# Performance work log

Measured on AMD Instinct MI355X. Metric: run time of the kernel, lower is better.

## Reference

```python
import jax, jax.numpy as jnp
import numpy as np

B, N, C = 16, 4096, 64
M, K, R = 1024, 32, 0.2
EPS = 1e-5  # BatchNorm eps (eval mode: running_mean=0, running_var=1)


def setup_inputs() -> dict:
    key = jax.random.key(0)
    ks = jax.random.split(key, 8)
    s = 0.05
    return {
        "points": jax.random.normal(ks[0], (B, 3, N), dtype=jnp.float32),
        "features": jax.random.normal(ks[1], (B, C, N), dtype=jnp.float32),
        "w1": jax.random.normal(ks[2], (64, 3 + C), dtype=jnp.float32) * s,
        "b1": jnp.zeros((64,), jnp.float32),
        "g1": jnp.ones((64,), jnp.float32),
        "be1": jnp.zeros((64,), jnp.float32),
        "w2": jax.random.normal(ks[3], (64, 64), dtype=jnp.float32) * s,
        "b2": jnp.zeros((64,), jnp.float32),
        "g2": jnp.ones((64,), jnp.float32),
        "be2": jnp.zeros((64,), jnp.float32),
        "w3": jax.random.normal(ks[4], (128, 64), dtype=jnp.float32) * s,
        "b3": jnp.zeros((128,), jnp.float32),
        "g3": jnp.ones((128,), jnp.float32),
        "be3": jnp.zeros((128,), jnp.float32),
    }


def farthest_point_sampling(pts, m):
    """pts: [B,N,3] -> indices [B,m] (iterative FPS, first point = index 0)."""
    b, n, _ = pts.shape

    def step(carry, _):
        dist, last = carry  # dist [b,n], last [b]
        lastp = jnp.take_along_axis(pts, last[:, None, None], axis=1)  # [b,1,3]
        d = jnp.sum((pts - lastp) ** 2, axis=-1)  # [b,n]
        dist = jnp.minimum(dist, d)
        nxt = jnp.argmax(dist, axis=1).astype(jnp.int32)
        return (dist, nxt), last

    init = (jnp.full((b, n), 1e10, pts.dtype), jnp.zeros((b,), jnp.int32))
    _, idx = jax.lax.scan(step, init, None, length=m)
    return idx.T  # [b,m]


def ball_query(pts, centroids, k, radius):
    """pts [B,N,3], centroids [B,M,3] -> neighbor indices [B,M,K].
    Takes the first k points (by index) within radius; pads with the first hit,
    matching the PointNet++ CUDA ball_query semantics."""
    n = pts.shape[1]
    p2 = jnp.sum(pts ** 2, -1)  # [B,N]
    c2 = jnp.sum(centroids ** 2, -1)  # [B,M]
    d2 = c2[:, :, None] + p2[:, None, :] - 2.0 * jnp.einsum("bmd,bnd->bmn", centroids, pts)
    ar = jnp.arange(n, dtype=jnp.int32)
    key = jnp.where(d2 <= radius * radius, ar[None, None, :], n)  # [B,M,N]
    idx = jnp.sort(key, axis=-1)[..., :k]  # first k in-radius indices (or n)
    first = idx[..., :1]  # centroid itself is always a hit (d2=0)
    idx = jnp.where(idx < n, idx, first)
    return jnp.clip(idx, 0, n - 1)


def _mlp_block(x, w, bias, g, be):
    # 1x1 Conv2d + BatchNorm (eval: mean=0, var=1) + ReLU, x: [B,M,K,Cin]
    y = jnp.einsum("oc,bmkc->bmko", w, x) + bias
    y = y * (g / jnp.sqrt(1.0 + EPS)) + be
    return jax.nn.relu(y)


def reference(points, features, w1, b1, g1, be1, w2, b2, g2, be2, w3, b3, g3, be3):
    pts = jnp.transpose(points, (0, 2, 1))  # [B,N,3]
    feats = jnp.transpose(features, (0, 2, 1))  # [B,N,C]
    b = pts.shape[0]

    cidx = farthest_point_sampling(pts, M)  # [B,M]
    bidx = jnp.arange(b)[:, None]
    cent = pts[bidx, cidx]  # [B,M,3]

    nidx = ball_query(pts, cent, K, R)  # [B,M,K]
    bidx2 = jnp.arange(b)[:, None, None]
    gpts = pts[bidx2, nidx]  # [B,M,K,3]
    gfeat = feats[bidx2, nidx]  # [B,M,K,C]
    local = gpts - cent[:, :, None, :]  # local coords
    x = jnp.concatenate([local, gfeat], axis=-1)  # [B,M,K,3+C]

    x = _mlp_block(x, w1, b1, g1, be1)
    x = _mlp_block(x, w2, b2, g2, be2)
    x = _mlp_block(x, w3, b3, g3, be3)

    out = jnp.max(x, axis=2)  # max over K samples -> [B,M,Cout]
    centroids = jnp.transpose(cent, (0, 2, 1))  # [B,3,M]
    out = jnp.transpose(out, (0, 2, 1))  # [B,Cout,M]
    return centroids, out
```

## Files before the change

kernel.cpp:

```cpp
#include <hip/hip_runtime.h>
#include <math.h>

#define NPTS 4096
#define MC   1024
#define KNB  32

typedef __attribute__((ext_vector_type(8))) short bf16x8;
typedef __attribute__((ext_vector_type(4))) float f32x4;

__device__ __forceinline__ unsigned short f2bf(float f) {
  unsigned int u = __float_as_uint(f);
  u = u + 0x7fffu + ((u >> 16) & 1u);
  return (unsigned short)(u >> 16);
}

template <int CTRL>
__device__ __forceinline__ float dpp_max(float v) {
  int o = __builtin_amdgcn_update_dpp(__float_as_int(v), __float_as_int(v), CTRL, 0xF, 0xF, false);
  return fmaxf(v, __int_as_float(o));
}

struct FpsShared {
  float sx[NPTS], sy[NPTS], sz[NPTS];
  unsigned long long skey[2][4];
  float slog[3][MC];
};
struct TransShared {
  float tile[64][65];
};

__global__ __launch_bounds__(256, 1) void fused_pre(
    const float* __restrict__ points, const float* __restrict__ feats,
    const float* __restrict__ w1, const float* __restrict__ w2,
    const float* __restrict__ w3,
    unsigned short* __restrict__ featsT, unsigned short* __restrict__ wpack,
    float* __restrict__ out_cent) {
  __shared__ union { FpsShared f; TransShared tr; } S;
  const int blk = blockIdx.x;
  const int t = threadIdx.x;

  if (blk < 16) {
    const int b = blk;
    const int w = t >> 6;
    const float* pb = points + (size_t)b * 3 * NPTS;

    float fx[16], fy[16], fz[16], dist[16];
#pragma unroll
    for (int k = 0; k < 4; ++k) {
      float4 X = ((const float4*)pb)[k * 256 + t];
      float4 Y = ((const float4*)(pb + NPTS))[k * 256 + t];
      float4 Z = ((const float4*)(pb + 2 * NPTS))[k * 256 + t];
      ((float4*)S.f.sx)[k * 256 + t] = X;
      ((float4*)S.f.sy)[k * 256 + t] = Y;
      ((float4*)S.f.sz)[k * 256 + t] = Z;
      fx[k * 4 + 0] = X.x; fx[k * 4 + 1] = X.y; fx[k * 4 + 2] = X.z; fx[k * 4 + 3] = X.w;
      fy[k * 4 + 0] = Y.x; fy[k * 4 + 1] = Y.y; fy[k * 4 + 2] = Y.z; fy[k * 4 + 3] = Y.w;
      fz[k * 4 + 0] = Z.x; fz[k * 4 + 1] = Z.y; fz[k * 4 + 2] = Z.z; fz[k * 4 + 3] = Z.w;
    }
#pragma unroll
    for (int j = 0; j < 16; ++j) dist[j] = 1e10f;
    __syncthreads();

    float lx = S.f.sx[0], ly = S.f.sy[0], lz = S.f.sz[0];

    for (int i = 0; i < MC; ++i) {
      if (t == 0) { S.f.slog[0][i] = lx; S.f.slog[1][i] = ly; S.f.slog[2][i] = lz; }
      if (i == MC - 1) break;

      float m = -1.0f;
#pragma unroll
      for (int j = 0; j < 16; ++j) {
        float dx = __fsub_rn(fx[j], lx);
        float dy = __fsub_rn(fy[j], ly);
        float dz = __fsub_rn(fz[j], lz);
        float d  = __fadd_rn(__fadd_rn(__fmul_rn(dx, dx), __fmul_rn(dy, dy)), __fmul_rn(dz, dz));
        float dm = fminf(dist[j], d);
        dist[j] = dm;
        m = fmaxf(m, dm);
      }

      m = dpp_max<0x111>(m);
      m = dpp_max<0x112>(m);
      m = dpp_max<0x114>(m);
      m = dpp_max<0x118>(m);
      m = dpp_max<0x142>(m);
      m = dpp_max<0x143>(m);
      const float wv = __int_as_float(__builtin_amdgcn_readlane(__float_as_int(m), 63));

      unsigned long long mk[4][4];
#pragma unroll
      for (int k = 0; k < 4; ++k) {
        mk[k][0] = __ballot(dist[k * 4 + 0] == wv);
        mk[k][1] = __ballot(dist[k * 4 + 1] == wv);
        mk[k][2] = __ballot(dist[k * 4 + 2] == wv);
        mk[k][3] = __ballot(dist[k * 4 + 3] == wv);
      }
      unsigned long long s0 = 0, s1 = 0, s2 = 0, s3 = 0, anyk = 0;
      int sk = -1;
#pragma unroll
      for (int k = 0; k < 4; ++k) {
        unsigned long long a = mk[k][0] | mk[k][1] | mk[k][2] | mk[k][3];
        if (sk < 0 && a != 0ull) {
          sk = k; anyk = a;
          s0 = mk[k][0]; s1 = mk[k][1]; s2 = mk[k][2]; s3 = mk[k][3];
        }
      }
      const int l = __builtin_ctzll(anyk);
      const unsigned long long bit = 1ull << l;
      const int c = (s0 & bit) ? 0 : (s1 & bit) ? 1 : (s2 & bit) ? 2 : 3;
      const int selIdx = sk * 1024 + 256 * w + 4 * l + c;

      const int nb = i & 1;
      if ((t & 63) == 0)
        S.f.skey[nb][w] = ((unsigned long long)__float_as_uint(wv) << 32) | (unsigned int)~selIdx;
      __syncthreads();

      unsigned long long k0 = S.f.skey[nb][0], k1 = S.f.skey[nb][1];
      unsigned long long k2 = S.f.skey[nb][2], k3 = S.f.skey[nb][3];
      unsigned long long ka = (k0 > k1) ? k0 : k1;
      unsigned long long kb = (k2 > k3) ? k2 : k3;
      unsigned long long km = (ka > kb) ? ka : kb;
      const int sel = (int)(~(unsigned int)km);
      lx = S.f.sx[sel]; ly = S.f.sy[sel]; lz = S.f.sz[sel];
    }
    __syncthreads();
    float* oc = out_cent + (size_t)b * 3 * MC;
#pragma unroll
    for (int k = 0; k < 12; ++k) {
      int idx = t + k * 256;
      oc[idx] = ((const float*)S.f.slog)[idx];
    }
  } else if (blk < 16 + 1024) {
    const int rel = blk - 16;
    const int b = rel >> 6;
    const int n0 = (rel & 63) * 64;
    const float* src = feats + (size_t)b * 64 * NPTS;
    {
      const int n = t & 63, cbase = t >> 6;
#pragma unroll
      for (int j = 0; j < 16; ++j) {
        int cc = cbase + j * 4;
        S.tr.tile[cc][n] = src[(size_t)cc * NPTS + n0 + n];
      }
    }
    __syncthreads();
    {
      const int cc = t & 63, nbase = t >> 6;
      unsigned short* dst = featsT + ((size_t)b * NPTS + n0) * 64;
#pragma unroll
      for (int j = 0; j < 16; ++j) {
        int n = nbase + j * 4;
        dst[(size_t)n * 64 + cc] = f2bf(S.tr.tile[cc][n]);
      }
    }
  } else {
    const int f = (blk - (16 + 1024)) * 4 + (t >> 6);
    const int lane = t & 63;
    if (f < 36) {
      int layer, kt, nt;
      if (f < 12)      { layer = 0; kt = f >> 2;        nt = f & 3; }
      else if (f < 20) { layer = 1; kt = (f - 12) >> 2; nt = (f - 12) & 3; }
      else             { layer = 2; kt = (f - 20) >> 3; nt = (f - 20) & 7; }
      const int o = nt * 16 + (lane & 15);
      unsigned short* dst = wpack + ((size_t)f * 64 + lane) * 8;
#pragma unroll
      for (int j = 0; j < 8; ++j) {
        int k = kt * 32 + (lane >> 4) * 8 + j;
        float x = 0.0f;
        if (layer == 0)      { if (k < 67) { int cin = (k < 64) ? (k + 3) : (k - 64); x = w1[o * 67 + cin]; } }
        else if (layer == 1) { x = w2[o * 64 + k]; }
        else                 { x = w3[o * 64 + k]; }
        dst[j] = f2bf(x);
      }
    }
  }
}

__global__ __launch_bounds__(256) void ball_query_kernel(const float* __restrict__ points,
                                                         const float* __restrict__ cent,
                                                         int* __restrict__ nidx) {
  __shared__ float sx[NPTS], sy[NPTS], sz[NPTS];
  __shared__ int lists[4][KNB];
  const int b  = blockIdx.x >> 4;
  const int cb = blockIdx.x & 15;
  const int t = threadIdx.x;
  const float* pb = points + (size_t)b * 3 * NPTS;
#pragma unroll
  for (int j = 0; j < 4; ++j) {
    int i4 = t + j * 256;
    ((float4*)sx)[i4] = ((const float4*)pb)[i4];
    ((float4*)sy)[i4] = ((const float4*)(pb + NPTS))[i4];
    ((float4*)sz)[i4] = ((const float4*)(pb + 2 * NPTS))[i4];
  }
  __syncthreads();
  const int w = t >> 6, lane = t & 63;
  const float R2 = (float)(0.2 * 0.2);
  const float* cbp = cent + (size_t)b * 3 * MC;
  for (int cm = 0; cm < 16; ++cm) {
    const int m  = cb * 64 + w * 16 + cm;
    const int bm = b * MC + m;
    const float cx = cbp[m], cy = cbp[MC + m], cz = cbp[2 * MC + m];
    const float c2 = __fadd_rn(__fadd_rn(__fmul_rn(cx, cx), __fmul_rn(cy, cy)), __fmul_rn(cz, cz));
    int cnt = 0;
    for (int ch = 0; ch < 64; ++ch) {
      const int n = ch * 64 + lane;
      float x = sx[n], y = sy[n], z = sz[n];
      float p2  = __fadd_rn(__fadd_rn(__fmul_rn(x, x),  __fmul_rn(y, y)),  __fmul_rn(z, z));
      float dot = __fadd_rn(__fadd_rn(__fmul_rn(cx, x), __fmul_rn(cy, y)), __fmul_rn(cz, z));
      float d2  = __fsub_rn(__fadd_rn(c2, p2), __fmul_rn(2.0f, dot));
      bool hit = (d2 <= R2);
      unsigned long long msk = __ballot(hit);
      if (hit) {
        int pos = cnt + __popcll(msk & ((1ull << lane) - 1ull));
        if (pos < KNB) lists[w][pos] = n;
      }
      cnt += __popcll(msk);
      if (cnt >= KNB) break;
    }
    if (lane < KNB) {
      int first = lists[w][0];
      int v = (lane < cnt) ? lists[w][lane] : first;
      nidx[(size_t)bm * KNB + lane] = v;
    }
  }
}

__global__ __launch_bounds__(256) void mlp_kernel(
    const float* __restrict__ points,
    const float* __restrict__ cent,
    const int* __restrict__ nidx,
    const unsigned short* __restrict__ featsT,
    const unsigned short* __restrict__ wpack,
    const float* __restrict__ b1, const float* __restrict__ g1, const float* __restrict__ be1,
    const float* __restrict__ b2, const float* __restrict__ g2, const float* __restrict__ be2,
    const float* __restrict__ b3, const float* __restrict__ g3, const float* __restrict__ be3,
    float* __restrict__ out) {
  __shared__ __align__(16) unsigned short Hs[4][2][32 * 72];
  __shared__ __align__(16) float obuf[128 * 20];
  const int t = threadIdx.x;
  const int w = t >> 6, lane = t & 63;
  const int r = lane & 15, q = lane >> 4;
  const float inv_s = 1.0f / sqrtf(1.0f + 1e-5f);

  float pb1[4], ps1[4], pe1[4], pb2[4], ps2[4], pe2[4], pb3[8], ps3[8], pe3[8];
#pragma unroll
  for (int nt = 0; nt < 4; ++nt) {
    int o = nt * 16 + r;
    pb1[nt] = b1[o]; ps1[nt] = g1[o] * inv_s; pe1[nt] = be1[o];
    pb2[nt] = b2[o]; ps2[nt] = g2[o] * inv_s; pe2[nt] = be2[o];
  }
#pragma unroll
  for (int nt = 0; nt < 8; ++nt) {
    int o = nt * 16 + r;
    pb3[nt] = b3[o]; ps3[nt] = g3[o] * inv_s; pe3[nt] = be3[o];
  }
  const int bm0 = blockIdx.x * 16;
  const int b   = bm0 >> 10;
  const int m0  = bm0 & 1023;
  const float* ptsb = points + (size_t)b * 3 * NPTS;
  const float* cbp  = cent + (size_t)b * 3 * MC;

  for (int it = 0; it < 4; ++it) {
    const int ml = it * 4 + w;
    const int bm = bm0 + ml;
    const int m  = bm & 1023;
    const int n0 = nidx[(size_t)bm * KNB + r];
    const int n1 = nidx[(size_t)bm * KNB + 16 + r];
    const float cx = cbp[m], cy = cbp[MC + m], cz = cbp[2 * MC + m];

    bf16x8 aF[2][2];
#pragma unroll
    for (int mt = 0; mt < 2; ++mt) {
      int n = mt ? n1 : n0;
      const unsigned short* rowp = featsT + ((size_t)b * NPTS + n) * 64 + q * 8;
      aF[mt][0] = *(const bf16x8*)(rowp);
      aF[mt][1] = *(const bf16x8*)(rowp + 32);
    }
    bf16x8 aL[2];
#pragma unroll
    for (int mt = 0; mt < 2; ++mt) {
      bf16x8 a = {0, 0, 0, 0, 0, 0, 0, 0};
      if (q == 0) {
        int n = mt ? n1 : n0;
        a[0] = (short)f2bf(ptsb[n] - cx);
        a[1] = (short)f2bf(ptsb[NPTS + n] - cy);
        a[2] = (short)f2bf(ptsb[2 * NPTS + n] - cz);
      }
      aL[mt] = a;
    }
    f32x4 acc1[2][4];
#pragma unroll
    for (int mt = 0; mt < 2; ++mt)
#pragma unroll
      for (int nt = 0; nt < 4; ++nt) acc1[mt][nt] = (f32x4){0.f, 0.f, 0.f, 0.f};
#pragma unroll
    for (int kt = 0; kt < 3; ++kt) {
#pragma unroll
      for (int nt = 0; nt < 4; ++nt) {
        bf16x8 wf = *(const bf16x8*)(wpack + ((size_t)(kt * 4 + nt) * 64 + lane) * 8);
#pragma unroll
        for (int mt = 0; mt < 2; ++mt) {
          bf16x8 a = (kt < 2) ? aF[mt][kt] : aL[mt];
          acc1[mt][nt] = __builtin_amdgcn_mfma_f32_16x16x32_bf16(a, wf, acc1[mt][nt], 0, 0, 0);
        }
      }
    }
#pragma unroll
    for (int mt = 0; mt < 2; ++mt)
#pragma unroll
      for (int nt = 0; nt < 4; ++nt)
#pragma unroll
        for (int rr = 0; rr < 4; ++rr) {
          float y = (acc1[mt][nt][rr] + pb1[nt]) * ps1[nt] + pe1[nt];
          y = fmaxf(y, 0.0f);
          Hs[w][0][(mt * 16 + q * 4 + rr) * 72 + nt * 16 + r] = f2bf(y);
        }
    __threadfence_block();

    f32x4 acc2[2][4];
#pragma unroll
    for (int mt = 0; mt < 2; ++mt)
#pragma unroll
      for (int nt = 0; nt < 4; ++nt) acc2[mt][nt] = (f32x4){0.f, 0.f, 0.f, 0.f};
#pragma unroll
    for (int kt = 0; kt < 2; ++kt) {
      bf16x8 a0 = *(const bf16x8*)&Hs[w][0][(0 * 16 + r) * 72 + kt * 32 + q * 8];
      bf16x8 a1 = *(const bf16x8*)&Hs[w][0][(1 * 16 + r) * 72 + kt * 32 + q * 8];
#pragma unroll
      for (int nt = 0; nt < 4; ++nt) {
        bf16x8 wf = *(const bf16x8*)(wpack + ((size_t)(12 + kt * 4 + nt) * 64 + lane) * 8);
        acc2[0][nt] = __builtin_amdgcn_mfma_f32_16x16x32_bf16(a0, wf, acc2[0][nt], 0, 0, 0);
        acc2[1][nt] = __builtin_amdgcn_mfma_f32_16x16x32_bf16(a1, wf, acc2[1][nt], 0, 0, 0);
      }
    }
#pragma unroll
    for (int mt = 0; mt < 2; ++mt)
#pragma unroll
      for (int nt = 0; nt < 4; ++nt)
#pragma unroll
        for (int rr = 0; rr < 4; ++rr) {
          float y = (acc2[mt][nt][rr] + pb2[nt]) * ps2[nt] + pe2[nt];
          y = fmaxf(y, 0.0f);
          Hs[w][1][(mt * 16 + q * 4 + rr) * 72 + nt * 16 + r] = f2bf(y);
        }
    __threadfence_block();

    f32x4 acc3[2][8];
#pragma unroll
    for (int mt = 0; mt < 2; ++mt)
#pragma unroll
      for (int nt = 0; nt < 8; ++nt) acc3[mt][nt] = (f32x4){0.f, 0.f, 0.f, 0.f};
#pragma unroll
    for (int kt = 0; kt < 2; ++kt) {
      bf16x8 a0 = *(const bf16x8*)&Hs[w][1][(0 * 16 + r) * 72 + kt * 32 + q * 8];
      bf16x8 a1 = *(const bf16x8*)&Hs[w][1][(1 * 16 + r) * 72 + kt * 32 + q * 8];
#pragma unroll
      for (int nt = 0; nt < 8; ++nt) {
        bf16x8 wf = *(const bf16x8*)(wpack + ((size_t)(20 + kt * 8 + nt) * 64 + lane) * 8);
        acc3[0][nt] = __builtin_amdgcn_mfma_f32_16x16x32_bf16(a0, wf, acc3[0][nt], 0, 0, 0);
        acc3[1][nt] = __builtin_amdgcn_mfma_f32_16x16x32_bf16(a1, wf, acc3[1][nt], 0, 0, 0);
      }
    }
#pragma unroll
    for (int nt = 0; nt < 8; ++nt) {
      float pm = 0.0f;
#pragma unroll
      for (int mt = 0; mt < 2; ++mt)
#pragma unroll
        for (int rr = 0; rr < 4; ++rr) {
          float y = (acc3[mt][nt][rr] + pb3[nt]) * ps3[nt] + pe3[nt];
          y = fmaxf(y, 0.0f);
          pm = fmaxf(pm, y);
        }
      pm = fmaxf(pm, __shfl_xor(pm, 16));
      pm = fmaxf(pm, __shfl_xor(pm, 32));
      if (q == 0) obuf[(nt * 16 + r) * 20 + ml] = pm;
    }
    __threadfence_block();
  }
  __syncthreads();
  {
    const int ch = t >> 1, mh = (t & 1) * 8;
    float4 u0 = *(const float4*)&obuf[ch * 20 + mh];
    float4 u1 = *(const float4*)&obuf[ch * 20 + mh + 4];
    float* outp = out + ((size_t)b * 128 + ch) * 1024 + m0 + mh;
    *(float4*)(outp)     = u0;
    *(float4*)(outp + 4) = u1;
  }
}

extern "C" void kernel_launch(void* const* d_in, const int* in_sizes, int n_in,
                              void* d_out, int out_size, void* d_ws, size_t ws_size,
                              hipStream_t stream) {
  (void)in_sizes; (void)n_in; (void)out_size; (void)ws_size;
  const float* points   = (const float*)d_in[0];
  const float* features = (const float*)d_in[1];
  const float* w1  = (const float*)d_in[2];
  const float* b1  = (const float*)d_in[3];
  const float* g1  = (const float*)d_in[4];
  const float* be1 = (const float*)d_in[5];
  const float* w2  = (const float*)d_in[6];
  const float* b2  = (const float*)d_in[7];
  const float* g2  = (const float*)d_in[8];
  const float* be2 = (const float*)d_in[9];
  const float* w3  = (const float*)d_in[10];
  const float* b3  = (const float*)d_in[11];
  const float* g3  = (const float*)d_in[12];
  const float* be3 = (const float*)d_in[13];

  float* outc = (float*)d_out;
  float* outf = outc + 16 * 3 * 1024;

  char* ws = (char*)d_ws;
  int*            nidx    = (int*)(ws);
  unsigned short* featsT  = (unsigned short*)(ws + 0x200000);
  unsigned short* wpack   = (unsigned short*)(ws + 0xA00000);

  fused_pre<<<16 + 1024 + 9, 256, 0, stream>>>(points, features, w1, w2, w3,
                                               featsT, wpack, outc);
  ball_query_kernel<<<256, 256, 0, stream>>>(points, outc, nidx);
  mlp_kernel<<<1024, 256, 0, stream>>>(points, outc, nidx, featsT, wpack,
                                       b1, g1, be1, b2, g2, be2, b3, g3, be3, outf);
}
```

Before: 979.7 us.

## Publish winner coordinates with FPS keys and use packed fp32 distance math

In the FPS loop, the winning lane of each wave now selects its own point coordinates from registers and writes them to shared memory next to its argmax key. After the barrier every thread picks the winning coordinates directly, so the dependent shared-memory lookup by index is gone and the full point copy in LDS is no longer needed. The distance computation is also rewritten with two-wide float vectors so the compiler can emit packed fp32 ops, with contraction disabled to keep rounding identical. The cost is a 16-way register select per iteration and a wider shared-memory write per wave.

```diff
diff --git a/kernel.cpp b/kernel.cpp
--- a/kernel.cpp
+++ b/kernel.cpp
@@ -7,6 +7,7 @@
 
 typedef __attribute__((ext_vector_type(8))) short bf16x8;
 typedef __attribute__((ext_vector_type(4))) float f32x4;
+typedef __attribute__((ext_vector_type(2))) float f32x2;
 
 __device__ __forceinline__ unsigned short f2bf(float f) {
   unsigned int u = __float_as_uint(f);
@@ -21,8 +22,8 @@
 }
 
 struct FpsShared {
-  float sx[NPTS], sy[NPTS], sz[NPTS];
   unsigned long long skey[2][4];
+  float4 scoord[2][4];
   float slog[3][MC];
 };
 struct TransShared {
@@ -41,7 +42,7 @@
 
   if (blk < 16) {
     const int b = blk;
-    const int w = t >> 6;
+    const int w = t >> 6, lane = t & 63;
     const float* pb = points + (size_t)b * 3 * NPTS;
 
     float fx[16], fy[16], fz[16], dist[16];
@@ -50,33 +51,40 @@
       float4 X = ((const float4*)pb)[k * 256 + t];
       float4 Y = ((const float4*)(pb + NPTS))[k * 256 + t];
       float4 Z = ((const float4*)(pb + 2 * NPTS))[k * 256 + t];
-      ((float4*)S.f.sx)[k * 256 + t] = X;
-      ((float4*)S.f.sy)[k * 256 + t] = Y;
-      ((float4*)S.f.sz)[k * 256 + t] = Z;
       fx[k * 4 + 0] = X.x; fx[k * 4 + 1] = X.y; fx[k * 4 + 2] = X.z; fx[k * 4 + 3] = X.w;
       fy[k * 4 + 0] = Y.x; fy[k * 4 + 1] = Y.y; fy[k * 4 + 2] = Y.z; fy[k * 4 + 3] = Y.w;
       fz[k * 4 + 0] = Z.x; fz[k * 4 + 1] = Z.y; fz[k * 4 + 2] = Z.z; fz[k * 4 + 3] = Z.w;
     }
 #pragma unroll
     for (int j = 0; j < 16; ++j) dist[j] = 1e10f;
-    __syncthreads();
-
-    float lx = S.f.sx[0], ly = S.f.sy[0], lz = S.f.sz[0];
+
+    float lx = pb[0], ly = pb[NPTS], lz = pb[2 * NPTS];
 
     for (int i = 0; i < MC; ++i) {
       if (t == 0) { S.f.slog[0][i] = lx; S.f.slog[1][i] = ly; S.f.slog[2][i] = lz; }
       if (i == MC - 1) break;
 
       float m = -1.0f;
-#pragma unroll
-      for (int j = 0; j < 16; ++j) {
-        float dx = __fsub_rn(fx[j], lx);
-        float dy = __fsub_rn(fy[j], ly);
-        float dz = __fsub_rn(fz[j], lz);
-        float d  = __fadd_rn(__fadd_rn(__fmul_rn(dx, dx), __fmul_rn(dy, dy)), __fmul_rn(dz, dz));
-        float dm = fminf(dist[j], d);
-        dist[j] = dm;
-        m = fmaxf(m, dm);
+      {
+#pragma clang fp contract(off)
+        const f32x2 Lx = (f32x2){lx, lx};
+        const f32x2 Ly = (f32x2){ly, ly};
+        const f32x2 Lz = (f32x2){lz, lz};
+#pragma unroll
+        for (int h = 0; h < 8; ++h) {
+          f32x2 px = (f32x2){fx[2 * h], fx[2 * h + 1]};
+          f32x2 py = (f32x2){fy[2 * h], fy[2 * h + 1]};
+          f32x2 pz = (f32x2){fz[2 * h], fz[2 * h + 1]};
+          f32x2 dx = px - Lx;
+          f32x2 dy = py - Ly;
+          f32x2 dz = pz - Lz;
+          f32x2 d = (dx * dx + dy * dy) + dz * dz;
+          float a0 = fminf(dist[2 * h], d.x);
+          float a1 = fminf(dist[2 * h + 1], d.y);
+          dist[2 * h] = a0;
+          dist[2 * h + 1] = a1;
+          m = fmaxf(m, fmaxf(a0, a1));
+        }
       }
 
       m = dpp_max<0x111>(m);
@@ -110,18 +118,34 @@
       const int c = (s0 & bit) ? 0 : (s1 & bit) ? 1 : (s2 & bit) ? 2 : 3;
       const int selIdx = sk * 1024 + 256 * w + 4 * l + c;
 
+      const int j_sel = sk * 4 + c;
+      float ex = fx[0], ey = fy[0], ez = fz[0];
+#pragma unroll
+      for (int j = 1; j < 16; ++j) {
+        const bool h = (j_sel == j);
+        ex = h ? fx[j] : ex;
+        ey = h ? fy[j] : ey;
+        ez = h ? fz[j] : ez;
+      }
+
       const int nb = i & 1;
-      if ((t & 63) == 0)
-        S.f.skey[nb][w] = ((unsigned long long)__float_as_uint(wv) << 32) | (unsigned int)~selIdx;
+      if (lane == l) {
+        S.f.skey[nb][w] =
+            ((unsigned long long)__float_as_uint(wv) << 32) | (unsigned int)~selIdx;
+        S.f.scoord[nb][w] = make_float4(ex, ey, ez, 0.0f);
+      }
       __syncthreads();
 
       unsigned long long k0 = S.f.skey[nb][0], k1 = S.f.skey[nb][1];
       unsigned long long k2 = S.f.skey[nb][2], k3 = S.f.skey[nb][3];
-      unsigned long long ka = (k0 > k1) ? k0 : k1;
-      unsigned long long kb = (k2 > k3) ? k2 : k3;
-      unsigned long long km = (ka > kb) ? ka : kb;
-      const int sel = (int)(~(unsigned int)km);
-      lx = S.f.sx[sel]; ly = S.f.sy[sel]; lz = S.f.sz[sel];
+      float4 c0 = S.f.scoord[nb][0], c1 = S.f.scoord[nb][1];
+      float4 c2 = S.f.scoord[nb][2], c3 = S.f.scoord[nb][3];
+      unsigned long long ka = k0; float4 ca = c0;
+      if (k1 > ka) { ka = k1; ca = c1; }
+      unsigned long long kb = k2; float4 cb = c2;
+      if (k3 > kb) { kb = k3; cb = c3; }
+      if (kb > ka) { ca = cb; }
+      lx = ca.x; ly = ca.y; lz = ca.z;
     }
     __syncthreads();
     float* oc = out_cent + (size_t)b * 3 * MC;
```

Measured after the change: 1.447 ms. +47.7%, slower.

## Fuse ball query into MLP kernel, keeping neighbor indices in registers

Applied to the files above, without the earlier changes.

Merges the ball query and MLP kernels into one: each block stages its batch's points into shared memory, computes neighbor lists for its 16 centroids, and builds the local coordinate inputs directly from shared memory. This removes one kernel launch, the global neighbor-index buffer round trip, and global gathers of point coordinates. In exchange every MLP block reloads all point coordinates for its batch, and the larger shared-memory union can limit occupancy.

```diff
diff --git a/kernel.cpp b/kernel.cpp
--- a/kernel.cpp
+++ b/kernel.cpp
@@ -176,35 +176,54 @@
   }
 }
 
-__global__ __launch_bounds__(256) void ball_query_kernel(const float* __restrict__ points,
-                                                         const float* __restrict__ cent,
-                                                         int* __restrict__ nidx) {
-  __shared__ float sx[NPTS], sy[NPTS], sz[NPTS];
+struct PtsS { float sx[NPTS], sy[NPTS], sz[NPTS]; };
+struct MlpS { unsigned short Hs[4][2][32 * 72]; float obuf[128 * 20]; };
+
+__global__ __launch_bounds__(256, 1) void mlp_bq_kernel(
+    const float* __restrict__ points,
+    const float* __restrict__ cent,
+    const unsigned short* __restrict__ featsT,
+    const unsigned short* __restrict__ wpack,
+    const float* __restrict__ b1, const float* __restrict__ g1, const float* __restrict__ be1,
+    const float* __restrict__ b2, const float* __restrict__ g2, const float* __restrict__ be2,
+    const float* __restrict__ b3, const float* __restrict__ g3, const float* __restrict__ be3,
+    float* __restrict__ out) {
+  __shared__ __align__(16) union { PtsS p; MlpS d; } U;
   __shared__ int lists[4][KNB];
-  const int b  = blockIdx.x >> 4;
-  const int cb = blockIdx.x & 15;
   const int t = threadIdx.x;
-  const float* pb = points + (size_t)b * 3 * NPTS;
-#pragma unroll
-  for (int j = 0; j < 4; ++j) {
-    int i4 = t + j * 256;
-    ((float4*)sx)[i4] = ((const float4*)pb)[i4];
-    ((float4*)sy)[i4] = ((const float4*)(pb + NPTS))[i4];
-    ((float4*)sz)[i4] = ((const float4*)(pb + 2 * NPTS))[i4];
+  const int w = t >> 6, lane = t & 63;
+  const int r = lane & 15, q = lane >> 4;
+  const float inv_s = 1.0f / sqrtf(1.0f + 1e-5f);
+
+  const int bm0 = blockIdx.x * 16;
+  const int b   = bm0 >> 10;
+  const int m0  = bm0 & 1023;
+  const float* cbp = cent + (size_t)b * 3 * MC;
+
+  {
+    const float* pb = points + (size_t)b * 3 * NPTS;
+#pragma unroll
+    for (int j = 0; j < 4; ++j) {
+      int i4 = t + j * 256;
+      ((float4*)U.p.sx)[i4] = ((const float4*)pb)[i4];
+      ((float4*)U.p.sy)[i4] = ((const float4*)(pb + NPTS))[i4];
+      ((float4*)U.p.sz)[i4] = ((const float4*)(pb + 2 * NPTS))[i4];
+    }
   }
   __syncthreads();
-  const int w = t >> 6, lane = t & 63;
+
+  int n0r[4], n1r[4];
+  bf16x8 aL[4][2];
   const float R2 = (float)(0.2 * 0.2);
-  const float* cbp = cent + (size_t)b * 3 * MC;
-  for (int cm = 0; cm < 16; ++cm) {
-    const int m  = cb * 64 + w * 16 + cm;
-    const int bm = b * MC + m;
+#pragma unroll
+  for (int it = 0; it < 4; ++it) {
+    const int m = m0 + it * 4 + w;
     const float cx = cbp[m], cy = cbp[MC + m], cz = cbp[2 * MC + m];
     const float c2 = __fadd_rn(__fadd_rn(__fmul_rn(cx, cx), __fmul_rn(cy, cy)), __fmul_rn(cz, cz));
     int cnt = 0;
     for (int ch = 0; ch < 64; ++ch) {
       const int n = ch * 64 + lane;
-      float x = sx[n], y = sy[n], z = sz[n];
+      float x = U.p.sx[n], y = U.p.sy[n], z = U.p.sz[n];
       float p2  = __fadd_rn(__fadd_rn(__fmul_rn(x, x),  __fmul_rn(y, y)),  __fmul_rn(z, z));
       float dot = __fadd_rn(__fadd_rn(__fmul_rn(cx, x), __fmul_rn(cy, y)), __fmul_rn(cz, z));
       float d2  = __fsub_rn(__fadd_rn(c2, p2), __fmul_rn(2.0f, dot));
@@ -217,30 +236,29 @@
       cnt += __popcll(msk);
       if (cnt >= KNB) break;
     }
-    if (lane < KNB) {
+    {
       int first = lists[w][0];
-      int v = (lane < cnt) ? lists[w][lane] : first;
-      nidx[(size_t)bm * KNB + lane] = v;
-    }
-  }
-}
-
-__global__ __launch_bounds__(256) void mlp_kernel(
-    const float* __restrict__ points,
-    const float* __restrict__ cent,
-    const int* __restrict__ nidx,
-    const unsigned short* __restrict__ featsT,
-    const unsigned short* __restrict__ wpack,
-    const float* __restrict__ b1, const float* __restrict__ g1, const float* __restrict__ be1,
-    const float* __restrict__ b2, const float* __restrict__ g2, const float* __restrict__ be2,
-    const float* __restrict__ b3, const float* __restrict__ g3, const float* __restrict__ be3,
-    float* __restrict__ out) {
-  __shared__ __align__(16) unsigned short Hs[4][2][32 * 72];
-  __shared__ __align__(16) float obuf[128 * 20];
-  const int t = threadIdx.x;
-  const int w = t >> 6, lane = t & 63;
-  const int r = lane & 15, q = lane >> 4;
-  const float inv_s = 1.0f / sqrtf(1.0f + 1e-5f);
+      if (lane < KNB) {
+        int v = (lane < cnt) ? lists[w][lane] : first;
+        lists[w][lane] = v;
+      }
+    }
+    const int n0 = lists[w][r];
+    const int n1 = lists[w][16 + r];
+    n0r[it] = n0; n1r[it] = n1;
+#pragma unroll
+    for (int mt = 0; mt < 2; ++mt) {
+      bf16x8 a = {0, 0, 0, 0, 0, 0, 0, 0};
+      if (q == 0) {
+        int n = mt ? n1 : n0;
+        a[0] = (short)f2bf(U.p.sx[n] - cx);
+        a[1] = (short)f2bf(U.p.sy[n] - cy);
+        a[2] = (short)f2bf(U.p.sz[n] - cz);
+      }
+      aL[it][mt] = a;
+    }
+  }
+  __syncthreads();
 
   float pb1[4], ps1[4], pe1[4], pb2[4], ps2[4], pe2[4], pb3[8], ps3[8], pe3[8];
 #pragma unroll
@@ -254,19 +272,10 @@
     int o = nt * 16 + r;
     pb3[nt] = b3[o]; ps3[nt] = g3[o] * inv_s; pe3[nt] = be3[o];
   }
-  const int bm0 = blockIdx.x * 16;
-  const int b   = bm0 >> 10;
-  const int m0  = bm0 & 1023;
-  const float* ptsb = points + (size_t)b * 3 * NPTS;
-  const float* cbp  = cent + (size_t)b * 3 * MC;
 
   for (int it = 0; it < 4; ++it) {
     const int ml = it * 4 + w;
-    const int bm = bm0 + ml;
-    const int m  = bm & 1023;
-    const int n0 = nidx[(size_t)bm * KNB + r];
-    const int n1 = nidx[(size_t)bm * KNB + 16 + r];
-    const float cx = cbp[m], cy = cbp[MC + m], cz = cbp[2 * MC + m];
+    const int n0 = n0r[it], n1 = n1r[it];
 
     bf16x8 aF[2][2];
 #pragma unroll
@@ -276,18 +285,6 @@
       aF[mt][0] = *(const bf16x8*)(rowp);
       aF[mt][1] = *(const bf16x8*)(rowp + 32);
     }
-    bf16x8 aL[2];
-#pragma unroll
-    for (int mt = 0; mt < 2; ++mt) {
-      bf16x8 a = {0, 0, 0, 0, 0, 0, 0, 0};
-      if (q == 0) {
-        int n = mt ? n1 : n0;
-        a[0] = (short)f2bf(ptsb[n] - cx);
-        a[1] = (short)f2bf(ptsb[NPTS + n] - cy);
-        a[2] = (short)f2bf(ptsb[2 * NPTS + n] - cz);
-      }
-      aL[mt] = a;
-    }
     f32x4 acc1[2][4];
 #pragma unroll
     for (int mt = 0; mt < 2; ++mt)
@@ -300,7 +297,7 @@
         bf16x8 wf = *(const bf16x8*)(wpack + ((size_t)(kt * 4 + nt) * 64 + lane) * 8);
 #pragma unroll
         for (int mt = 0; mt < 2; ++mt) {
-          bf16x8 a = (kt < 2) ? aF[mt][kt] : aL[mt];
+          bf16x8 a = (kt < 2) ? aF[mt][kt] : aL[it][mt];
           acc1[mt][nt] = __builtin_amdgcn_mfma_f32_16x16x32_bf16(a, wf, acc1[mt][nt], 0, 0, 0);
         }
       }
@@ -313,7 +310,7 @@
         for (int rr = 0; rr < 4; ++rr) {
           float y = (acc1[mt][nt][rr] + pb1[nt]) * ps1[nt] + pe1[nt];
           y = fmaxf(y, 0.0f);
-          Hs[w][0][(mt * 16 + q * 4 + rr) * 72 + nt * 16 + r] = f2bf(y);
+          U.d.Hs[w][0][(mt * 16 + q * 4 + rr) * 72 + nt * 16 + r] = f2bf(y);
         }
     __threadfence_block();
 
@@ -324,8 +321,8 @@
       for (int nt = 0; nt < 4; ++nt) acc2[mt][nt] = (f32x4){0.f, 0.f, 0.f, 0.f};
 #pragma unroll
     for (int kt = 0; kt < 2; ++kt) {
-      bf16x8 a0 = *(const bf16x8*)&Hs[w][0][(0 * 16 + r) * 72 + kt * 32 + q * 8];
-      bf16x8 a1 = *(const bf16x8*)&Hs[w][0][(1 * 16 + r) * 72 + kt * 32 + q * 8];
+      bf16x8 a0 = *(const bf16x8*)&U.d.Hs[w][0][(0 * 16 + r) * 72 + kt * 32 + q * 8];
+      bf16x8 a1 = *(const bf16x8*)&U.d.Hs[w][0][(1 * 16 + r) * 72 + kt * 32 + q * 8];
 #pragma unroll
       for (int nt = 0; nt < 4; ++nt) {
         bf16x8 wf = *(const bf16x8*)(wpack + ((size_t)(12 + kt * 4 + nt) * 64 + lane) * 8);
@@ -341,7 +338,7 @@
         for (int rr = 0; rr < 4; ++rr) {
           float y = (acc2[mt][nt][rr] + pb2[nt]) * ps2[nt] + pe2[nt];
           y = fmaxf(y, 0.0f);
-          Hs[w][1][(mt * 16 + q * 4 + rr) * 72 + nt * 16 + r] = f2bf(y);
+          U.d.Hs[w][1][(mt * 16 + q * 4 + rr) * 72 + nt * 16 + r] = f2bf(y);
         }
     __threadfence_block();
 
@@ -352,8 +349,8 @@
       for (int nt = 0; nt < 8; ++nt) acc3[mt][nt] = (f32x4){0.f, 0.f, 0.f, 0.f};
 #pragma unroll
     for (int kt = 0; kt < 2; ++kt) {
-      bf16x8 a0 = *(const bf16x8*)&Hs[w][1][(0 * 16 + r) * 72 + kt * 32 + q * 8];
-      bf16x8 a1 = *(const bf16x8*)&Hs[w][1][(1 * 16 + r) * 72 + kt * 32 + q * 8];
+      bf16x8 a0 = *(const bf16x8*)&U.d.Hs[w][1][(0 * 16 + r) * 72 + kt * 32 + q * 8];
+      bf16x8 a1 = *(const bf16x8*)&U.d.Hs[w][1][(1 * 16 + r) * 72 + kt * 32 + q * 8];
 #pragma unroll
       for (int nt = 0; nt < 8; ++nt) {
         bf16x8 wf = *(const bf16x8*)(wpack + ((size_t)(20 + kt * 8 + nt) * 64 + lane) * 8);
@@ -374,15 +371,15 @@
         }
       pm = fmaxf(pm, __shfl_xor(pm, 16));
       pm = fmaxf(pm, __shfl_xor(pm, 32));
-      if (q == 0) obuf[(nt * 16 + r) * 20 + ml] = pm;
+      if (q == 0) U.d.obuf[(nt * 16 + r) * 20 + ml] = pm;
     }
     __threadfence_block();
   }
   __syncthreads();
   {
     const int ch = t >> 1, mh = (t & 1) * 8;
-    float4 u0 = *(const float4*)&obuf[ch * 20 + mh];
-    float4 u1 = *(const float4*)&obuf[ch * 20 + mh + 4];
+    float4 u0 = *(const float4*)&U.d.obuf[ch * 20 + mh];
+    float4 u1 = *(const float4*)&U.d.obuf[ch * 20 + mh + 4];
     float* outp = out + ((size_t)b * 128 + ch) * 1024 + m0 + mh;
     *(float4*)(outp)     = u0;
     *(float4*)(outp + 4) = u1;
@@ -412,13 +409,12 @@
   float* outf = outc + 16 * 3 * 1024;
 
   char* ws = (char*)d_ws;
-  int*            nidx    = (int*)(ws);
-  unsigned short* featsT  = (unsigned short*)(ws + 0x200000);
-  unsigned short* wpack   = (unsigned short*)(ws + 0xA00000);
+  unsigned short* featsT  = (unsigned short*)(ws);
+  unsigned short* wpack   = (unsigned short*)(ws + 0x800000);
 
   fused_pre<<<16 + 1024 + 9, 256, 0, stream>>>(points, features, w1, w2, w3,
                                                featsT, wpack, outc);
-  ball_query_kernel<<<256, 256, 0, stream>>>(points, outc, nidx);
-  mlp_kernel<<<1024, 256, 0, stream>>>(points, outc, nidx, featsT, wpack,
-                                       b1, g1, be1, b2, g2, be2, b3, g3, be3, outf);
+  mlp_bq_kernel<<<1024, 256, 0, stream>>>(points, outc, featsT, wpack,
+                                          b1, g1, be1, b2, g2, be2,
+                                          b3, g3, be3, outf);
 }
```

After: 1.060 ms. 8.2% more time.
